# Optimization experiments

Hardware: AMD Instinct MI355X
Metric: run time of the kernel (lower is better)

## Reference

```python
import jax, jax.numpy as jnp
import numpy as np

N = 100_000
E = 3_200_000
P = 128
K = 128


def setup_inputs() -> dict:
    key = jax.random.key(0)
    ks = jax.random.split(key, 12)

    def xavier(k, shape):
        fan_in, fan_out = shape[1], shape[0]
        lim = jnp.sqrt(6.0 / (fan_in + fan_out))
        return jax.random.uniform(k, shape, jnp.float32, -lim, lim)

    return {
        "s_v": jax.random.normal(ks[0], (N,), jnp.float32),
        "t_v": jax.random.normal(ks[1], (N,), jnp.float32),
        "x": jax.random.normal(ks[2], (N, K), jnp.float32),
        "edge_src": jax.random.randint(ks[3], (E,), 0, N),
        "edge_dst": jax.random.randint(ks[4], (E,), 0, N),
        "theta1": xavier(ks[5], (P, 2)),
        "theta2": xavier(ks[6], (P, K)),
        "theta3": xavier(ks[7], (2 * P, 1)),
        "theta4": xavier(ks[8], (P, P)),
        "theta5": xavier(ks[9], (P, P)),
        "h_theta": xavier(ks[10], (P, 2 * P)),
    }


def reference(s_v, t_v, x, edge_src, edge_dst, theta1, theta2, theta3, theta4, theta5, h_theta):
    n = x.shape[0]
    # per-node embedding: mu_v = relu(theta1 @ conn + theta2 @ x_v_normalized)
    conn = jnp.stack([s_v, t_v], axis=1)                      # [N, 2]
    norm = jnp.linalg.norm(x, axis=1, keepdims=True)          # [N, 1]
    xn = x / jnp.where(norm == 0, 1.0, norm)
    mu = jax.nn.relu(conn @ theta1.T + xn @ theta2.T)         # [N, P]
    # neighbor-difference sum: s_v = deg(v)*mu_v - sum_{u in N(v)} mu_u
    ones = jnp.ones(edge_src.shape, mu.dtype)
    deg = jax.ops.segment_sum(ones, edge_src, num_segments=n)           # [N]
    nb_sum = jax.ops.segment_sum(mu[edge_dst], edge_src, num_segments=n)  # [N, P]
    s = deg[:, None] * mu - nb_sum
    # mu' = h_theta @ relu([mu; s])
    mu_prime = jax.nn.relu(jnp.concatenate([mu, s], axis=1)) @ h_theta.T  # [N, P]
    sum_mu_prime = mu_prime.sum(axis=0)                        # [P]
    # Q_v = theta3^T relu([theta4 @ sum_mu'; theta5 @ mu'_v])
    up = theta4 @ sum_mu_prime                                 # [P], shared
    down = mu_prime @ theta5.T                                 # [N, P]
    z = jax.nn.relu(jnp.concatenate([jnp.broadcast_to(up, (n, up.shape[0])), down], axis=1))
    return z @ theta3                                          # [N, 1]
```

## Files before the change

kernel.cpp:

```cpp
#include <hip/hip_runtime.h>
#include <stdint.h>

typedef unsigned int uint;
typedef unsigned short ushort;
typedef __attribute__((ext_vector_type(4))) float f32x4;
typedef __attribute__((ext_vector_type(2))) float f32x2;
typedef __attribute__((ext_vector_type(8))) short bf16x8;

union U4H8 { uint4 u; bf16x8 h; };

__device__ __forceinline__ float bflo(uint u){ return __uint_as_float(u << 16); }
__device__ __forceinline__ float bfhi(uint u){ return __uint_as_float(u & 0xffff0000u); }
__device__ __forceinline__ ushort f2bf(float f){
  uint u = __float_as_uint(f);
  return (ushort)((u + 0x7fffu + ((u >> 16) & 1u)) >> 16);
}
__device__ __forceinline__ uint pack2(float lo, float hi){
  return ((uint)f2bf(hi) << 16) | (uint)f2bf(lo);
}

__device__ __forceinline__ uint fp8e(float f){
  uint u = __float_as_uint(f);
  uint r = u + 0x7FFFFu + ((u >> 20) & 1u);
  uint code = (((r >> 23) - 120u) << 3) | ((r >> 20) & 7u);
  code = (code > 0x7Eu) ? 0x7Eu : code;
  uint den = (uint)__float2int_rn(f * 512.0f);
  return (f >= 0.015625f) ? code : den;
}

__device__ __forceinline__ void fp8acc(float* acc, uint w, int off){
  f32x2 lo = __builtin_amdgcn_cvt_pk_f32_fp8(w, false);
  f32x2 hi = __builtin_amdgcn_cvt_pk_f32_fp8(w, true);
  acc[off+0] += lo[0]; acc[off+1] += lo[1];
  acc[off+2] += hi[0]; acc[off+3] += hi[1];
}

#define CHUNK 8192
#define GGRID 2048
#define REDB  64

__global__ __launch_bounds__(256) void k_mu(
    const float* __restrict__ x, const float* __restrict__ sv,
    const float* __restrict__ tv, const float* __restrict__ th1,
    const float* __restrict__ th2, ushort* __restrict__ mu_s,
    uint2* __restrict__ mu8, int n)
{
  __shared__ uint4 B[2048];
  const int tid = threadIdx.x;
  for (int f = tid; f < 2048; f += 256) {
    int l = f & 63, rest = f >> 6;
    int s = rest >> 3, t = rest & 7;
    int row = t*16 + (l & 15);
    int kb  = s*32 + (l >> 4)*8;
    const float* p = th2 + row*128 + kb;
    float4 a = *(const float4*)p;
    float4 b = *(const float4*)(p + 4);
    uint4 u; u.x = pack2(a.x,a.y); u.y = pack2(a.z,a.w);
    u.z = pack2(b.x,b.y); u.w = pack2(b.z,b.w);
    B[(s*8 + t)*64 + l] = u;
  }
  __syncthreads();
  const int w = tid >> 6, l = tid & 63, q = l >> 4, c = l & 15;
  float2 t1[8];
  #pragma unroll
  for (int t = 0; t < 8; ++t) t1[t] = ((const float2*)th1)[t*16 + c];
  const int ntiles = (n + 15) >> 4;
  for (int T = blockIdx.x*4 + w; T < ntiles; T += gridDim.x*4) {
    int v0 = T*16;
    int arow = min(v0 + c, n-1);
    const float4* xr = (const float4*)(x + (size_t)arow*128);
    float4 xf[8];
    #pragma unroll
    for (int s = 0; s < 4; ++s) {
      xf[2*s]   = xr[s*8 + q*2];
      xf[2*s+1] = xr[s*8 + q*2 + 1];
    }
    float ss = 0.f;
    #pragma unroll
    for (int i = 0; i < 8; ++i)
      ss += xf[i].x*xf[i].x + xf[i].y*xf[i].y + xf[i].z*xf[i].z + xf[i].w*xf[i].w;
    ss += __shfl_xor(ss, 16, 64);
    ss += __shfl_xor(ss, 32, 64);
    float inv = (ss > 0.f) ? rsqrtf(ss) : 1.f;
    U4H8 a[4];
    #pragma unroll
    for (int s = 0; s < 4; ++s) {
      float4 u0 = xf[2*s], u1 = xf[2*s+1];
      a[s].u = make_uint4(pack2(u0.x*inv, u0.y*inv), pack2(u0.z*inv, u0.w*inv),
                          pack2(u1.x*inv, u1.y*inv), pack2(u1.z*inv, u1.w*inv));
    }
    f32x4 acc[8];
    #pragma unroll
    for (int t = 0; t < 8; ++t) acc[t] = (f32x4){0.f,0.f,0.f,0.f};
    #pragma unroll
    for (int s = 0; s < 4; ++s) {
      #pragma unroll
      for (int t = 0; t < 8; ++t) {
        U4H8 b; b.u = B[(s*8 + t)*64 + l];
        acc[t] = __builtin_amdgcn_mfma_f32_16x16x32_bf16(a[s].h, b.h, acc[t], 0, 0, 0);
      }
    }
    float svr[4], tvr[4];
    #pragma unroll
    for (int r = 0; r < 4; ++r) {
      int node = min(v0 + q*4 + r, n-1);
      svr[r] = sv[node]; tvr[r] = tv[node];
    }
    #pragma unroll
    for (int r = 0; r < 4; ++r) {
      int node = v0 + q*4 + r;
      if (node < n) {
        float mm[8];
        #pragma unroll
        for (int t = 0; t < 8; ++t) {
          mm[t] = fmaxf(acc[t][r] + t1[t].x*svr[r] + t1[t].y*tvr[r], 0.f);
          mu_s[(size_t)node*128 + t*16 + c] = f2bf(mm[t]);
        }
        uint u0 = fp8e(mm[0]) | (fp8e(mm[1]) << 8) |
                  (fp8e(mm[2]) << 16) | (fp8e(mm[3]) << 24);
        uint u1 = fp8e(mm[4]) | (fp8e(mm[5]) << 8) |
                  (fp8e(mm[6]) << 16) | (fp8e(mm[7]) << 24);
        mu8[(size_t)node*16 + c] = make_uint2(u0, u1);
      }
    }
  }
}

__global__ __launch_bounds__(256) void k_m2(const float* __restrict__ th5,
    const float* __restrict__ hth, float* __restrict__ M2)
{
  __shared__ float row[128];
  const int r = blockIdx.x, j = threadIdx.x;
  if (j < 128) row[j] = th5[r*128 + j];
  __syncthreads();
  float acc = 0.f;
  #pragma unroll 8
  for (int k = 0; k < 128; ++k) acc += row[k] * hth[k*256 + j];
  M2[r*256 + j] = acc;
}


__global__ __launch_bounds__(256) void k_hist(const int* __restrict__ src,
    int* __restrict__ histG, int e, int nblk)
{
  __shared__ int lh[256];
  const int blk = blockIdx.x, tid = threadIdx.x;
  lh[tid] = 0; __syncthreads();
  const int lo = blk*CHUNK, hi = min(e, lo + CHUNK);
  for (int i = lo + tid; i < hi; i += 256)
    atomicAdd(&lh[src[i] >> 9], 1);
  __syncthreads();
  histG[tid*nblk + blk] = lh[tid];
}

__global__ __launch_bounds__(512) void k_scanH(int* __restrict__ histG,
    int* __restrict__ bucketTot, int nblk)
{
  __shared__ int tmp[512];
  const int b = blockIdx.x, tid = threadIdx.x;
  int v = (tid < nblk) ? histG[b*nblk + tid] : 0;
  tmp[tid] = v; __syncthreads();
  for (int off = 1; off < 512; off <<= 1) {
    int t = (tid >= off) ? tmp[tid - off] : 0;
    __syncthreads();
    tmp[tid] += t;
    __syncthreads();
  }
  if (tid < nblk) histG[b*nblk + tid] = tmp[tid] - v;
  if (tid == nblk - 1) bucketTot[b] = tmp[tid];
}

__global__ __launch_bounds__(256) void k_scanB(const int* __restrict__ bucketTot,
    int* __restrict__ bucketBase)
{
  __shared__ int tmp[256];
  int tid = threadIdx.x;
  int v = bucketTot[tid];
  tmp[tid] = v; __syncthreads();
  for (int off = 1; off < 256; off <<= 1) {
    int t = (tid >= off) ? tmp[tid - off] : 0;
    __syncthreads();
    tmp[tid] += t;
    __syncthreads();
  }
  bucketBase[tid] = tmp[tid] - v;
}

__global__ __launch_bounds__(256) void k_part(
    const int* __restrict__ src, const int* __restrict__ dst,
    const int* __restrict__ histG, const int* __restrict__ bucketBase,
    uint* __restrict__ packed, int e, int nblk)
{
  __shared__ int cur[256];
  const int blk = blockIdx.x, tid = threadIdx.x;
  cur[tid] = bucketBase[tid] + histG[tid*nblk + blk];
  __syncthreads();
  const int lo = blk*CHUNK, hi = min(e, lo + CHUNK);
  for (int i = lo + tid; i < hi; i += 256) {
    int s = src[i], d = dst[i];
    int pos = atomicAdd(&cur[s >> 9], 1);
    packed[pos] = ((uint)(s & 511) << 17) | (uint)d;
  }
}

__global__ __launch_bounds__(512) void k_csr(
    const uint* __restrict__ packed, const int* __restrict__ bucketTot,
    const int* __restrict__ bucketBase, int* __restrict__ sorted,
    int* __restrict__ rowstart, int* __restrict__ cnt, int n)
{
  __shared__ int lc[512];
  __shared__ int lofs[512];
  __shared__ int lcur[512];
  const int b = blockIdx.x, tid = threadIdx.x;
  const int base = bucketBase[b], tot = bucketTot[b];
  lc[tid] = 0; __syncthreads();
  for (int i = tid; i < tot; i += 512)
    atomicAdd(&lc[packed[base + i] >> 17], 1);
  __syncthreads();
  lofs[tid] = lc[tid]; __syncthreads();
  for (int off = 1; off < 512; off <<= 1) {
    int t = (tid >= off) ? lofs[tid - off] : 0;
    __syncthreads();
    lofs[tid] += t;
    __syncthreads();
  }
  int excl = lofs[tid] - lc[tid];
  int node = (b << 9) + tid;
  lcur[tid] = base + excl;
  if (node < n) { rowstart[node] = base + excl; cnt[node] = lc[tid]; }
  __syncthreads();
  for (int i = tid; i < tot; i += 512) {
    uint p = packed[base + i];
    int pos = atomicAdd(&lcur[p >> 17], 1);
    sorted[pos] = (int)(p & 0x1FFFFu);
  }
}

__global__ __launch_bounds__(256) void k_gather(
    const uint4* __restrict__ mu8, const uint* __restrict__ mu_u,
    const int* __restrict__ sorted, const int* __restrict__ cnt,
    const int* __restrict__ rowstart, uint* __restrict__ rs_u,
    float* __restrict__ part, int n)
{
  __shared__ float ls[4*256];
  const int w = threadIdx.x >> 6, l = threadIdx.x & 63;
  const int g = l >> 3, c = l & 7;
  float cm0 = 0.f, cm1 = 0.f, cr0 = 0.f, cr1 = 0.f;
  for (int v = blockIdx.x*4 + w; v < n; v += gridDim.x*4) {
    int deg = cnt[v], start = rowstart[v];
    float acc[16];
    #pragma unroll
    for (int i = 0; i < 16; ++i) acc[i] = 0.f;
    for (int base = 0; base < deg; base += 64) {
      int m = min(deg - base, 64);
      int idx = (l < m) ? sorted[start + base + l] : 0;
      int full = m & ~7;
      for (int j = 0; j < full; j += 8) {
        int d = __shfl(idx, j + g, 64);
        uint4 u = mu8[(size_t)d*8 + c];
        fp8acc(acc, u.x, 0); fp8acc(acc, u.y, 4);
        fp8acc(acc, u.z, 8); fp8acc(acc, u.w, 12);
      }
      int rem = m - full;
      if (rem) {
        int d = __shfl(idx, full + min(g, rem-1), 64);
        if (g < rem) {
          uint4 u = mu8[(size_t)d*8 + c];
          fp8acc(acc, u.x, 0); fp8acc(acc, u.y, 4);
          fp8acc(acc, u.z, 8); fp8acc(acc, u.w, 12);
        }
      }
    }
    uint um = mu_u[(size_t)v*64 + l];
    #pragma unroll
    for (int i = 0; i < 16; ++i) {
      acc[i] += __shfl_xor(acc[i], 8, 64);
      acc[i] += __shfl_xor(acc[i], 16, 64);
      acc[i] += __shfl_xor(acc[i], 32, 64);
    }
    float a01 = (g & 1) ? acc[1] : acc[0];
    float a23 = (g & 1) ? acc[3] : acc[2];
    float a45 = (g & 1) ? acc[5] : acc[4];
    float a67 = (g & 1) ? acc[7] : acc[6];
    float b01 = (g & 1) ? acc[9]  : acc[8];
    float b23 = (g & 1) ? acc[11] : acc[10];
    float b45 = (g & 1) ? acc[13] : acc[12];
    float b67 = (g & 1) ? acc[15] : acc[14];
    float a03 = (g & 2) ? a23 : a01;
    float a47 = (g & 2) ? a67 : a45;
    float b03 = (g & 2) ? b23 : b01;
    float b47 = (g & 2) ? b67 : b45;
    float alo = (g & 4) ? a47 : a03;
    float ahi = (g & 4) ? b47 : b03;
    float m0 = bflo(um), m1 = bfhi(um);
    float dg = (float)deg;
    float s0 = fmaxf(dg*m0 - alo, 0.f);
    float s1 = fmaxf(dg*m1 - ahi, 0.f);
    rs_u[(size_t)v*64 + l] = pack2(s0, s1);
    cm0 += m0; cm1 += m1;
    cr0 += s0; cr1 += s1;
  }
  ls[w*256 + 2*l]         = cm0;
  ls[w*256 + 2*l + 1]     = cm1;
  ls[w*256 + 128 + 2*l]   = cr0;
  ls[w*256 + 128 + 2*l+1] = cr1;
  __syncthreads();
  int tid = threadIdx.x;
  part[(size_t)blockIdx.x*256 + tid] =
      ls[tid] + ls[256+tid] + ls[512+tid] + ls[768+tid];
}

__global__ __launch_bounds__(256) void k_red(const float* __restrict__ part,
    float* __restrict__ part2)
{
  const int t = threadIdx.x, b = blockIdx.x;
  const int rpb = GGRID / REDB;
  float s = 0.f;
  for (int r = b*rpb; r < b*rpb + rpb; ++r) s += part[(size_t)r*256 + t];
  part2[(size_t)b*256 + t] = s;
}

__global__ __launch_bounds__(128) void k_upC(const float* __restrict__ part,
    int npart, const float* __restrict__ hth, const float* __restrict__ th4,
    const float* __restrict__ th3, float* __restrict__ Cbuf) {
  __shared__ float Q[256];
  __shared__ float S[128];
  __shared__ float pr[128];
  int tid = threadIdx.x;
  float q0 = 0.f, q1 = 0.f;
  for (int b = 0; b < npart; ++b) {
    q0 += part[(size_t)b*256 + tid];
    q1 += part[(size_t)b*256 + 128 + tid];
  }
  Q[tid] = q0; Q[128 + tid] = q1;
  __syncthreads();
  float gs = 0.f;
  const float4* hr = (const float4*)(hth + tid*256);
  const float4* Q4 = (const float4*)Q;
  #pragma unroll 8
  for (int k = 0; k < 64; ++k) {
    float4 a = hr[k], b = Q4[k];
    gs += a.x*b.x + a.y*b.y + a.z*b.z + a.w*b.w;
  }
  S[tid] = gs;
  __syncthreads();
  float up = 0.f;
  const float4* r4 = (const float4*)(th4 + tid*128);
  const float4* S4 = (const float4*)S;
  #pragma unroll 8
  for (int k = 0; k < 32; ++k) {
    float4 a = r4[k], b = S4[k];
    up += a.x*b.x + a.y*b.y + a.z*b.z + a.w*b.w;
  }
  float r = th3[tid] * fmaxf(up, 0.f);
  pr[tid] = r; __syncthreads();
  if (tid < 64) pr[tid] += pr[tid + 64];
  __syncthreads();
  if (tid < 64) {
    float v = pr[tid];
    #pragma unroll
    for (int off = 32; off > 0; off >>= 1) v += __shfl_down(v, off, 64);
    if (tid == 0) Cbuf[0] = v;
  }
}

__global__ __launch_bounds__(256) void k_out(
    const uint4* __restrict__ mu4, const uint4* __restrict__ rs4,
    const float* __restrict__ M2, const float* __restrict__ th3,
    const float* __restrict__ Cbuf, float* __restrict__ out, int n)
{
  __shared__ uint4 B[4096];
  const int tid = threadIdx.x;
  for (int f = tid; f < 4096; f += 256) {
    int l = f & 63, rest = f >> 6;
    int s = rest >> 3, t = rest & 7;
    int row = t*16 + (l & 15);
    int kb  = s*32 + (l >> 4)*8;
    const float* p = M2 + row*256 + kb;
    float4 a = *(const float4*)p;
    float4 b = *(const float4*)(p + 4);
    uint4 u; u.x = pack2(a.x,a.y); u.y = pack2(a.z,a.w);
    u.z = pack2(b.x,b.y); u.w = pack2(b.z,b.w);
    B[(s*8 + t)*64 + l] = u;
  }
  __syncthreads();
  const int w = tid >> 6, l = tid & 63, q = l >> 4, c = l & 15;
  float t3w[8];
  #pragma unroll
  for (int t = 0; t < 8; ++t) t3w[t] = th3[128 + t*16 + c];
  const float C = Cbuf[0];
  const int ntiles = (n + 15) >> 4;
  for (int T = blockIdx.x*4 + w; T < ntiles; T += gridDim.x*4) {
    int v0 = T*16;
    int arow = min(v0 + c, n-1);
    U4H8 a[8];
    #pragma unroll
    for (int s = 0; s < 4; ++s) a[s].u   = mu4[(size_t)arow*16 + s*4 + q];
    #pragma unroll
    for (int s = 0; s < 4; ++s) a[4+s].u = rs4[(size_t)arow*16 + s*4 + q];
    f32x4 acc[8];
    #pragma unroll
    for (int t = 0; t < 8; ++t) acc[t] = (f32x4){0.f,0.f,0.f,0.f};
    #pragma unroll
    for (int s = 0; s < 8; ++s) {
      #pragma unroll
      for (int t = 0; t < 8; ++t) {
        U4H8 b; b.u = B[(s*8 + t)*64 + l];
        acc[t] = __builtin_amdgcn_mfma_f32_16x16x32_bf16(a[s].h, b.h, acc[t], 0, 0, 0);
      }
    }
    float red[4] = {0.f, 0.f, 0.f, 0.f};
    #pragma unroll
    for (int t = 0; t < 8; ++t) {
      #pragma unroll
      for (int r = 0; r < 4; ++r)
        red[r] += t3w[t] * fmaxf(acc[t][r], 0.f);
    }
    #pragma unroll
    for (int r = 0; r < 4; ++r) {
      #pragma unroll
      for (int off = 1; off < 16; off <<= 1)
        red[r] += __shfl_xor(red[r], off, 64);
    }
    if (c == 0) {
      #pragma unroll
      for (int r = 0; r < 4; ++r) {
        int node = v0 + q*4 + r;
        if (node < n) out[node] = C + red[r];
      }
    }
  }
}

extern "C" void kernel_launch(void* const* d_in, const int* in_sizes, int n_in,
                              void* d_out, int out_size, void* d_ws, size_t ws_size,
                              hipStream_t stream)
{
  const float* sv  = (const float*)d_in[0];
  const float* tv  = (const float*)d_in[1];
  const float* x   = (const float*)d_in[2];
  const int*   esrc= (const int*)d_in[3];
  const int*   edst= (const int*)d_in[4];
  const float* th1 = (const float*)d_in[5];
  const float* th2 = (const float*)d_in[6];
  const float* th3 = (const float*)d_in[7];
  const float* th4 = (const float*)d_in[8];
  const float* th5 = (const float*)d_in[9];
  const float* hth = (const float*)d_in[10];
  float* out = (float*)d_out;
  const int n = in_sizes[0];
  const int e = in_sizes[3];

  const int nblk  = (e + CHUNK - 1) / CHUNK;
  const int nbuck = (n + 511) >> 9;

  char* wp = (char*)d_ws;
  auto carve = [&](size_t bytes) { char* p = wp; wp += (bytes + 255) & ~(size_t)255; return p; };
  char*   R1    = (char*) carve((size_t)n*128*2);
  ushort* mu_s  = (ushort*)carve((size_t)n*128*2);
  ushort* rs_s  = (ushort*)carve((size_t)n*128*2);
  int*    sorted= (int*)   carve((size_t)e*4);
  int*    cnt   = (int*)   carve((size_t)n*4);
  int*    rowst = (int*)   carve((size_t)n*4);
  int*    histG = (int*)   carve((size_t)256*nblk*4);
  int*    btot  = (int*)   carve(256*4);
  int*    bbase = (int*)   carve(256*4);
  float*  M2    = (float*) carve(128*256*4);
  float*  part  = (float*) carve((size_t)GGRID*256*4);
  float*  part2 = (float*) carve((size_t)REDB*256*4);
  float*  Cbuf  = (float*) carve(256);

  uint*   packed= (uint*)R1;
  uint2*  mu8   = (uint2*)(R1 + (size_t)n*128);

  k_mu    <<<1024, 256, 0, stream>>>(x, sv, tv, th1, th2, mu_s, mu8, n);
  k_m2    <<<128, 256, 0, stream>>>(th5, hth, M2);
  k_hist  <<<nblk, 256, 0, stream>>>(esrc, histG, e, nblk);
  k_scanH <<<256, 512, 0, stream>>>(histG, btot, nblk);
  k_scanB <<<1, 256, 0, stream>>>(btot, bbase);
  k_part  <<<nblk, 256, 0, stream>>>(esrc, edst, histG, bbase, packed, e, nblk);
  k_csr   <<<nbuck, 512, 0, stream>>>(packed, btot, bbase, sorted, rowst, cnt, n);
  k_gather<<<GGRID, 256, 0, stream>>>((const uint4*)mu8, (const uint*)mu_s,
                                      sorted, cnt, rowst, (uint*)rs_s, part, n);
  k_red   <<<REDB, 256, 0, stream>>>(part, part2);
  k_upC   <<<1, 128, 0, stream>>>(part2, REDB, hth, th4, th3, Cbuf);
  k_out   <<<1024, 256, 0, stream>>>((const uint4*)mu_s, (const uint4*)rs_s,
                                     M2, th3, Cbuf, out, n);
}
```

Baseline: 374.2 us.

## Build CSR with global per-node atomic counting instead of two-level bucket sort

Replaces the two-pass bucketed partition (local histograms, bucket partition, per-bucket CSR) with a direct scheme: global atomic degree counts per node, block sums and scans to get row starts, then a fill pass using global atomics on per-node cursors. This removes the intermediate packed buffer and one full pass over the edges. The cost is 3.2M global atomics, issued twice, on random addresses, and the order of neighbours within each row becomes nondeterministic.

```diff
diff --git a/kernel.cpp b/kernel.cpp
--- a/kernel.cpp
+++ b/kernel.cpp
@@ -35,7 +35,6 @@
   acc[off+2] += hi[0]; acc[off+3] += hi[1];
 }
 
-#define CHUNK 8192
 #define GGRID 2048
 #define REDB  64
 
@@ -140,34 +139,29 @@
 }
 
 
-__global__ __launch_bounds__(256) void k_hist(const int* __restrict__ src,
-    int* __restrict__ histG, int e, int nblk)
-{
-  __shared__ int lh[256];
-  const int blk = blockIdx.x, tid = threadIdx.x;
-  lh[tid] = 0; __syncthreads();
-  const int lo = blk*CHUNK, hi = min(e, lo + CHUNK);
-  for (int i = lo + tid; i < hi; i += 256)
-    atomicAdd(&lh[src[i] >> 9], 1);
-  __syncthreads();
-  histG[tid*nblk + blk] = lh[tid];
-}
-
-__global__ __launch_bounds__(512) void k_scanH(int* __restrict__ histG,
-    int* __restrict__ bucketTot, int nblk)
-{
-  __shared__ int tmp[512];
-  const int b = blockIdx.x, tid = threadIdx.x;
-  int v = (tid < nblk) ? histG[b*nblk + tid] : 0;
-  tmp[tid] = v; __syncthreads();
-  for (int off = 1; off < 512; off <<= 1) {
-    int t = (tid >= off) ? tmp[tid - off] : 0;
+__global__ __launch_bounds__(256) void k_cnt(const int* __restrict__ src,
+    int* __restrict__ cnt, int e)
+{
+  int i = blockIdx.x*256 + threadIdx.x;
+  const int stride = gridDim.x*256;
+  for (; i < e; i += stride)
+    atomicAdd(&cnt[src[i]], 1);
+}
+
+__global__ __launch_bounds__(256) void k_bsum(const int* __restrict__ cnt,
+    int* __restrict__ btot, int n)
+{
+  __shared__ int s[256];
+  const int b = blockIdx.x, t = threadIdx.x;
+  const int base = b*512;
+  int v0 = (base + t       < n) ? cnt[base + t]       : 0;
+  int v1 = (base + 256 + t < n) ? cnt[base + 256 + t] : 0;
+  s[t] = v0 + v1; __syncthreads();
+  for (int off = 128; off > 0; off >>= 1) {
+    if (t < off) s[t] += s[t + off];
     __syncthreads();
-    tmp[tid] += t;
-    __syncthreads();
-  }
-  if (tid < nblk) histG[b*nblk + tid] = tmp[tid] - v;
-  if (tid == nblk - 1) bucketTot[b] = tmp[tid];
+  }
+  if (t == 0) btot[b] = s[0];
 }
 
 __global__ __launch_bounds__(256) void k_scanB(const int* __restrict__ bucketTot,
@@ -186,53 +180,39 @@
   bucketBase[tid] = tmp[tid] - v;
 }
 
-__global__ __launch_bounds__(256) void k_part(
-    const int* __restrict__ src, const int* __restrict__ dst,
-    const int* __restrict__ histG, const int* __restrict__ bucketBase,
-    uint* __restrict__ packed, int e, int nblk)
-{
-  __shared__ int cur[256];
-  const int blk = blockIdx.x, tid = threadIdx.x;
-  cur[tid] = bucketBase[tid] + histG[tid*nblk + blk];
-  __syncthreads();
-  const int lo = blk*CHUNK, hi = min(e, lo + CHUNK);
-  for (int i = lo + tid; i < hi; i += 256) {
+__global__ __launch_bounds__(512) void k_nodescan(const int* __restrict__ cnt,
+    const int* __restrict__ bbase, int* __restrict__ rowstart,
+    int* __restrict__ cur, int n)
+{
+  __shared__ int lofs[512];
+  const int b = blockIdx.x, t = threadIdx.x;
+  const int node = b*512 + t;
+  int c = (node < n) ? cnt[node] : 0;
+  lofs[t] = c; __syncthreads();
+  for (int off = 1; off < 512; off <<= 1) {
+    int x = (t >= off) ? lofs[t - off] : 0;
+    __syncthreads();
+    lofs[t] += x;
+    __syncthreads();
+  }
+  int excl = lofs[t] - c;
+  if (node < n) {
+    int rs = bbase[b] + excl;
+    rowstart[node] = rs;
+    cur[node] = rs;
+  }
+}
+
+__global__ __launch_bounds__(256) void k_fill(const int* __restrict__ src,
+    const int* __restrict__ dst, int* __restrict__ cur,
+    int* __restrict__ sorted, int e)
+{
+  int i = blockIdx.x*256 + threadIdx.x;
+  const int stride = gridDim.x*256;
+  for (; i < e; i += stride) {
     int s = src[i], d = dst[i];
-    int pos = atomicAdd(&cur[s >> 9], 1);
-    packed[pos] = ((uint)(s & 511) << 17) | (uint)d;
-  }
-}
-
-__global__ __launch_bounds__(512) void k_csr(
-    const uint* __restrict__ packed, const int* __restrict__ bucketTot,
-    const int* __restrict__ bucketBase, int* __restrict__ sorted,
-    int* __restrict__ rowstart, int* __restrict__ cnt, int n)
-{
-  __shared__ int lc[512];
-  __shared__ int lofs[512];
-  __shared__ int lcur[512];
-  const int b = blockIdx.x, tid = threadIdx.x;
-  const int base = bucketBase[b], tot = bucketTot[b];
-  lc[tid] = 0; __syncthreads();
-  for (int i = tid; i < tot; i += 512)
-    atomicAdd(&lc[packed[base + i] >> 17], 1);
-  __syncthreads();
-  lofs[tid] = lc[tid]; __syncthreads();
-  for (int off = 1; off < 512; off <<= 1) {
-    int t = (tid >= off) ? lofs[tid - off] : 0;
-    __syncthreads();
-    lofs[tid] += t;
-    __syncthreads();
-  }
-  int excl = lofs[tid] - lc[tid];
-  int node = (b << 9) + tid;
-  lcur[tid] = base + excl;
-  if (node < n) { rowstart[node] = base + excl; cnt[node] = lc[tid]; }
-  __syncthreads();
-  for (int i = tid; i < tot; i += 512) {
-    uint p = packed[base + i];
-    int pos = atomicAdd(&lcur[p >> 17], 1);
-    sorted[pos] = (int)(p & 0x1FFFFu);
+    int pos = atomicAdd(&cur[s], 1);
+    sorted[pos] = d;
   }
 }
 
@@ -451,7 +431,6 @@
   const int n = in_sizes[0];
   const int e = in_sizes[3];
 
-  const int nblk  = (e + CHUNK - 1) / CHUNK;
   const int nbuck = (n + 511) >> 9;
 
   char* wp = (char*)d_ws;
@@ -462,7 +441,7 @@
   int*    sorted= (int*)   carve((size_t)e*4);
   int*    cnt   = (int*)   carve((size_t)n*4);
   int*    rowst = (int*)   carve((size_t)n*4);
-  int*    histG = (int*)   carve((size_t)256*nblk*4);
+  int*    cur   = (int*)   carve((size_t)n*4);
   int*    btot  = (int*)   carve(256*4);
   int*    bbase = (int*)   carve(256*4);
   float*  M2    = (float*) carve(128*256*4);
@@ -470,16 +449,16 @@
   float*  part2 = (float*) carve((size_t)REDB*256*4);
   float*  Cbuf  = (float*) carve(256);
 
-  uint*   packed= (uint*)R1;
   uint2*  mu8   = (uint2*)(R1 + (size_t)n*128);
 
+  hipMemsetAsync(cnt, 0, (size_t)n*4, stream);
   k_mu    <<<1024, 256, 0, stream>>>(x, sv, tv, th1, th2, mu_s, mu8, n);
   k_m2    <<<128, 256, 0, stream>>>(th5, hth, M2);
-  k_hist  <<<nblk, 256, 0, stream>>>(esrc, histG, e, nblk);
-  k_scanH <<<256, 512, 0, stream>>>(histG, btot, nblk);
+  k_cnt   <<<2048, 256, 0, stream>>>(esrc, cnt, e);
+  k_bsum  <<<256, 256, 0, stream>>>(cnt, btot, n);
   k_scanB <<<1, 256, 0, stream>>>(btot, bbase);
-  k_part  <<<nblk, 256, 0, stream>>>(esrc, edst, histG, bbase, packed, e, nblk);
-  k_csr   <<<nbuck, 512, 0, stream>>>(packed, btot, bbase, sorted, rowst, cnt, n);
+  k_nodescan<<<nbuck, 512, 0, stream>>>(cnt, bbase, rowst, cur, n);
+  k_fill  <<<2048, 256, 0, stream>>>(esrc, edst, cur, sorted, e);
   k_gather<<<GGRID, 256, 0, stream>>>((const uint4*)mu8, (const uint*)mu_s,
                                       sorted, cnt, rowst, (uint*)rs_s, part, n);
   k_red   <<<REDB, 256, 0, stream>>>(part, part2);
```

New measurement: 698.1 us. +86.6%, slower.
